# Optimization experiments

Hardware: AMD Instinct MI355X
Metric: run time of the kernel (lower is better)

The kernel has to match this reference:

```python
import jax, jax.numpy as jnp
import numpy as np

N, K = 50000, 10      # nodes, sampled neighbors (num_sample)
V, F = 200000, 128    # embedding table rows, input_dim
H = 64                # hidden per direction (hidden_dim=128, bidirectional)


def setup_inputs() -> dict:
    key = jax.random.key(0)
    ks = jax.random.split(key, 12)
    s = 1.0 / np.sqrt(H)  # torch LSTM init: U(-1/sqrt(H), 1/sqrt(H))
    u = lambda k, shape: jax.random.uniform(k, shape, jnp.float32, -s, s)
    return {
        "neigh_idx": jax.random.randint(ks[0], (N, K), 0, V),
        "embed_table": jax.random.normal(ks[1], (V, F), jnp.float32) * 0.02,
        # forward-direction LSTM params (torch gate order: i, f, g, o)
        "Wih_f": u(ks[2], (4 * H, F)), "Whh_f": u(ks[3], (4 * H, H)),
        "bih_f": u(ks[4], (4 * H,)),   "bhh_f": u(ks[5], (4 * H,)),
        # backward-direction LSTM params
        "Wih_b": u(ks[6], (4 * H, F)), "Whh_b": u(ks[7], (4 * H, H)),
        "bih_b": u(ks[8], (4 * H,)),   "bhh_b": u(ks[9], (4 * H,)),
    }


def _lstm_scan(x, Wih, Whh, bih, bhh):
    """x: [N,K,F] -> hidden outputs [N,K,H] (single direction)."""
    n = x.shape[0]
    # precompute input projections for all steps: [N,K,4H]
    xg = jnp.einsum('nkf,gf->nkg', x, Wih) + bih + bhh
    h0 = jnp.zeros((n, H), x.dtype)
    c0 = jnp.zeros((n, H), x.dtype)

    def step(carry, xt):
        h, c = carry
        gates = xt + h @ Whh.T
        i, f, g, o = jnp.split(gates, 4, axis=-1)
        i = jax.nn.sigmoid(i)
        f = jax.nn.sigmoid(f)
        g = jnp.tanh(g)
        o = jax.nn.sigmoid(o)
        c = f * c + i * g
        h = o * jnp.tanh(c)
        return (h, c), h

    _, hs = jax.lax.scan(step, (h0, c0), jnp.swapaxes(xg, 0, 1))  # [K,N,H]
    return jnp.swapaxes(hs, 0, 1)


def reference(neigh_idx, embed_table, Wih_f, Whh_f, bih_f, bhh_f,
              Wih_b, Whh_b, bih_b, bhh_b):
    x = embed_table[neigh_idx]  # gather: [N,K,F]
    # forward direction: last-step hidden
    h_f = _lstm_scan(x, Wih_f, Whh_f, bih_f, bhh_f)[:, -1, :]
    # backward direction processes reversed sequence; torch output[:, -1] of the
    # backward stream is its hidden after processing only element K-1 (step 0).
    h_b = _lstm_scan(x[:, ::-1, :], Wih_b, Whh_b, bih_b, bhh_b)[:, 0, :]
    return jnp.concatenate([h_f, h_b], axis=-1)  # [N, 2H]
```

## Files before the change

kernel.cpp:

```cpp
#include <hip/hip_runtime.h>
#include <hip/hip_bf16.h>


#define NN 50000
#define KK 10
#define FF 128
#define HH 64

#define WS_WIH_F 0
#define WS_WHH_F 32768
#define WS_WIH_B 49152

#define NPB 32
#define HS 72

typedef __bf16 bf16x8 __attribute__((ext_vector_type(8)));
typedef float f32x4 __attribute__((ext_vector_type(4)));

__device__ __forceinline__ float fast_sig(float x) {
    float e = exp2f(x * -1.44269504f);
    return __builtin_amdgcn_rcpf(1.0f + e);
}
__device__ __forceinline__ float fast_tanh(float x) {
    float xx = fminf(fmaxf(x, -15.0f), 15.0f);
    float e = exp2f(xx * 2.88539008f);
    return (e - 1.0f) * __builtin_amdgcn_rcpf(e + 1.0f);
}

__global__ void cvt_weights_kernel(const float* __restrict__ Wih_f,
                                   const float* __restrict__ Whh_f,
                                   const float* __restrict__ Wih_b,
                                   __bf16* __restrict__ ws) {
    int i = blockIdx.x * 256 + threadIdx.x;
    ws[WS_WIH_F + i] = (__bf16)Wih_f[i];
    if (i < 16384) ws[WS_WHH_F + i] = (__bf16)Whh_f[i];
    ws[WS_WIH_B + i] = (__bf16)Wih_b[i];
}

__global__ __launch_bounds__(256, 2) void lstm_agg_kernel(
    const int* __restrict__ nidx,
    const float* __restrict__ tab,
    const float* __restrict__ bih_f,
    const float* __restrict__ bhh_f,
    const float* __restrict__ bih_b,
    const float* __restrict__ bhh_b,
    const __bf16* __restrict__ ws,
    float* __restrict__ out)
{
    __shared__ float  x_lds[2][NPB * FF];
    __shared__ __bf16 h_lds[2][NPB * HS];
    __shared__ int    gq[NPB][KK];

    const int tid  = threadIdx.x;
    const int w    = tid >> 6;
    const int lane = tid & 63;
    const int q    = lane >> 4;
    const int c    = lane & 15;
    const int koff = q * 8;
    const int half = lane >> 5;
    const int l31  = lane & 31;
    const int node_base = blockIdx.x * NPB;
    const int sw = (c & 7) << 4;

    for (int i = tid; i < NPB * KK; i += 256) {
        int r = i / KK, k = i - r * KK;
        int node = min(node_base + r, NN - 1);
        gq[r][k] = nidx[node * KK + k];
    }

    auto stage = [&](int b, int kidx) {
#pragma unroll
        for (int j = 0; j < 4; ++j) {
            const int R = w * 8 + 2 * j + half;
            const int g = gq[R][kidx];
            const char* src = (const char*)tab + (size_t)g * 512
                              + ((l31 ^ (R & 7)) << 4);
            float* dst = &x_lds[b][(w * 8 + 2 * j) * FF];
            __builtin_amdgcn_global_load_lds(
                (const __attribute__((address_space(1))) void*)src,
                (__attribute__((address_space(3))) void*)dst, 16, 0, 0);
        }
    };

    __syncthreads();
    stage(0, 0);

    bf16x8 bWih[4][4], bWhh[4][2];
#pragma unroll
    for (int g = 0; g < 4; ++g) {
        int row = (g * 4 + w) * 16 + c;
#pragma unroll
        for (int kk = 0; kk < 4; ++kk)
            bWih[g][kk] = *(const bf16x8*)(ws + WS_WIH_F + row * FF + kk * 32 + koff);
#pragma unroll
        for (int kk = 0; kk < 2; ++kk)
            bWhh[g][kk] = *(const bf16x8*)(ws + WS_WHH_F + row * HH + kk * 32 + koff);
    }
    float bias[4];
#pragma unroll
    for (int g = 0; g < 4; ++g) {
        int u = g * 64 + w * 16 + c;
        bias[g] = bih_f[u] + bhh_f[u];
    }

    __syncthreads();

    f32x4 acc[4][2];
    float cst[2][4];
#pragma unroll
    for (int r = 0; r < 2; ++r)
#pragma unroll
        for (int e = 0; e < 4; ++e) cst[r][e] = 0.0f;

    for (int k = 0; k < KK; ++k) {
        const int cur = k & 1;
        if (k + 1 < KK) stage(cur ^ 1, k + 1);

#pragma unroll
        for (int g = 0; g < 4; ++g)
#pragma unroll
            for (int r = 0; r < 2; ++r)
                acc[g][r] = (f32x4){bias[g], bias[g], bias[g], bias[g]};

        const char* xb = (const char*)x_lds[cur];
#pragma unroll
        for (int r = 0; r < 2; ++r) {
            const char* rp = xb + (r * 16 + c) * 512;
            bf16x8 xa[4];
#pragma unroll
            for (int kk = 0; kk < 4; ++kk) {
                const int base = kk * 128 + q * 32;
                f32x4 lo = *(const f32x4*)(rp + ((base) ^ sw));
                f32x4 hi = *(const f32x4*)(rp + ((base + 16) ^ sw));
                bf16x8 v;
#pragma unroll
                for (int e = 0; e < 4; ++e) {
                    v[e]     = (__bf16)lo[e];
                    v[4 + e] = (__bf16)hi[e];
                }
                xa[kk] = v;
            }
#pragma unroll
            for (int g = 0; g < 4; ++g)
#pragma unroll
                for (int kk = 0; kk < 4; ++kk)
                    acc[g][r] = __builtin_amdgcn_mfma_f32_16x16x32_bf16(
                        xa[kk], bWih[g][kk], acc[g][r], 0, 0, 0);
        }

        if (k > 0) {
            const __bf16* hb = h_lds[(k - 1) & 1];
#pragma unroll
            for (int r = 0; r < 2; ++r) {
                bf16x8 ha[2];
#pragma unroll
                for (int kk = 0; kk < 2; ++kk)
                    ha[kk] = *(const bf16x8*)(hb + (r * 16 + c) * HS + kk * 32 + koff);
#pragma unroll
                for (int g = 0; g < 4; ++g)
#pragma unroll
                    for (int kk = 0; kk < 2; ++kk)
                        acc[g][r] = __builtin_amdgcn_mfma_f32_16x16x32_bf16(
                            ha[kk], bWhh[g][kk], acc[g][r], 0, 0, 0);
            }
        }

        const bool last = (k == KK - 1);
        __bf16* hw = h_lds[k & 1];
#pragma unroll
        for (int r = 0; r < 2; ++r)
#pragma unroll
            for (int reg = 0; reg < 4; ++reg) {
                float gi = fast_sig(acc[0][r][reg]);
                float gf = fast_sig(acc[1][r][reg]);
                float gg = fast_tanh(acc[2][r][reg]);
                float go = fast_sig(acc[3][r][reg]);
                float cn = gf * cst[r][reg] + gi * gg;
                cst[r][reg] = cn;
                float h = go * fast_tanh(cn);
                hw[(r * 16 + q * 4 + reg) * HS + w * 16 + c] = (__bf16)h;
                if (last) {
                    int node = node_base + r * 16 + q * 4 + reg;
                    if (node < NN) out[(size_t)node * 128 + w * 16 + c] = h;
                }
            }
        __syncthreads();
    }

    {
        const int gb[3] = {0, 2, 3};
        bf16x8 bW[3][4];
        float  bb[3];
#pragma unroll
        for (int j = 0; j < 3; ++j) {
            int row = (gb[j] * 4 + w) * 16 + c;
#pragma unroll
            for (int kk = 0; kk < 4; ++kk)
                bW[j][kk] = *(const bf16x8*)(ws + WS_WIH_B + row * FF + kk * 32 + koff);
            int u = gb[j] * 64 + w * 16 + c;
            bb[j] = bih_b[u] + bhh_b[u];
        }
        const char* xb = (const char*)x_lds[(KK - 1) & 1];
#pragma unroll
        for (int r = 0; r < 2; ++r) {
            f32x4 a0 = (f32x4){bb[0], bb[0], bb[0], bb[0]};
            f32x4 a1 = (f32x4){bb[1], bb[1], bb[1], bb[1]};
            f32x4 a2 = (f32x4){bb[2], bb[2], bb[2], bb[2]};
            const char* rp = xb + (r * 16 + c) * 512;
            bf16x8 xa[4];
#pragma unroll
            for (int kk = 0; kk < 4; ++kk) {
                const int base = kk * 128 + q * 32;
                f32x4 lo = *(const f32x4*)(rp + ((base) ^ sw));
                f32x4 hi = *(const f32x4*)(rp + ((base + 16) ^ sw));
                bf16x8 v;
#pragma unroll
                for (int e = 0; e < 4; ++e) {
                    v[e]     = (__bf16)lo[e];
                    v[4 + e] = (__bf16)hi[e];
                }
                xa[kk] = v;
            }
#pragma unroll
            for (int kk = 0; kk < 4; ++kk) {
                a0 = __builtin_amdgcn_mfma_f32_16x16x32_bf16(xa[kk], bW[0][kk], a0, 0, 0, 0);
                a1 = __builtin_amdgcn_mfma_f32_16x16x32_bf16(xa[kk], bW[1][kk], a1, 0, 0, 0);
                a2 = __builtin_amdgcn_mfma_f32_16x16x32_bf16(xa[kk], bW[2][kk], a2, 0, 0, 0);
            }
#pragma unroll
            for (int reg = 0; reg < 4; ++reg) {
                float gi = fast_sig(a0[reg]);
                float gg = fast_tanh(a1[reg]);
                float go = fast_sig(a2[reg]);
                float hb2 = go * fast_tanh(gi * gg);
                int node = node_base + r * 16 + q * 4 + reg;
                if (node < NN) out[(size_t)node * 128 + 64 + w * 16 + c] = hb2;
            }
        }
    }
}

extern "C" void kernel_launch(void* const* d_in, const int* in_sizes, int n_in,
                              void* d_out, int out_size, void* d_ws, size_t ws_size,
                              hipStream_t stream) {
    const int*   nidx  = (const int*)d_in[0];
    const float* tab   = (const float*)d_in[1];
    const float* Wih_f = (const float*)d_in[2];
    const float* Whh_f = (const float*)d_in[3];
    const float* bih_f = (const float*)d_in[4];
    const float* bhh_f = (const float*)d_in[5];
    const float* Wih_b = (const float*)d_in[6];
    const float* bih_b = (const float*)d_in[8];
    const float* bhh_b = (const float*)d_in[9];
    __bf16* ws  = (__bf16*)d_ws;
    float*  out = (float*)d_out;

    hipLaunchKernelGGL(cvt_weights_kernel, dim3(32768 / 256), dim3(256), 0, stream,
                       Wih_f, Whh_f, Wih_b, ws);

    const int blocks = (NN + NPB - 1) / NPB;
    hipLaunchKernelGGL(lstm_agg_kernel, dim3(blocks), dim3(256), 0, stream,
                       nidx, tab, bih_f, bhh_f, bih_b, bhh_b, ws, out);
}
```

Measured before the change: 274.7 us.

## Stage gathered embeddings through registers and store bf16 in LDS

Replaces the direct global-to-LDS async copy of fp32 embedding rows with register loads that are converted to bf16 once and written to a swizzled bf16 LDS buffer after the step's compute. This halves LDS footprint and read traffic, and removes the repeated fp32-to-bf16 conversion on every MFMA operand read, which may allow higher occupancy. In exchange the gather now holds 16 extra VGPRs across the step and needs explicit VALU stores, so load latency is hidden only by the compute between load and write.

```diff
diff --git a/kernel.cpp b/kernel.cpp
--- a/kernel.cpp
+++ b/kernel.cpp
@@ -47,7 +47,7 @@
     const __bf16* __restrict__ ws,
     float* __restrict__ out)
 {
-    __shared__ float  x_lds[2][NPB * FF];
+    __shared__ __bf16 x_lds[2][NPB * FF];
     __shared__ __bf16 h_lds[2][NPB * HS];
     __shared__ int    gq[NPB][KK];
 
@@ -57,10 +57,12 @@
     const int q    = lane >> 4;
     const int c    = lane & 15;
     const int koff = q * 8;
-    const int half = lane >> 5;
-    const int l31  = lane & 31;
     const int node_base = blockIdx.x * NPB;
     const int sw = (c & 7) << 4;
+
+    const int srow  = tid >> 3;
+    const int spart = tid & 7;
+    const int swW   = (srow & 7) << 4;
 
     for (int i = tid; i < NPB * KK; i += 256) {
         int r = i / KK, k = i - r * KK;
@@ -68,22 +70,28 @@
         gq[r][k] = nidx[node * KK + k];
     }
 
-    auto stage = [&](int b, int kidx) {
-#pragma unroll
-        for (int j = 0; j < 4; ++j) {
-            const int R = w * 8 + 2 * j + half;
-            const int g = gq[R][kidx];
-            const char* src = (const char*)tab + (size_t)g * 512
-                              + ((l31 ^ (R & 7)) << 4);
-            float* dst = &x_lds[b][(w * 8 + 2 * j) * FF];
-            __builtin_amdgcn_global_load_lds(
-                (const __attribute__((address_space(1))) void*)src,
-                (__attribute__((address_space(3))) void*)dst, 16, 0, 0);
-        }
+    f32x4 G[4];
+    auto stage_load = [&](int kidx) {
+        const float* src = tab + (size_t)gq[srow][kidx] * FF + spart * 16;
+#pragma unroll
+        for (int j = 0; j < 4; ++j) G[j] = *(const f32x4*)(src + j * 4);
     };
+    auto stage_write = [&](int b) {
+        bf16x8 v0, v1;
+#pragma unroll
+        for (int e = 0; e < 4; ++e) {
+            v0[e]     = (__bf16)G[0][e];
+            v0[4 + e] = (__bf16)G[1][e];
+            v1[e]     = (__bf16)G[2][e];
+            v1[4 + e] = (__bf16)G[3][e];
+        }
+        char* row = (char*)(x_lds[b] + srow * FF);
+        *(bf16x8*)(row + ((spart * 32)      ^ swW)) = v0;
+        *(bf16x8*)(row + ((spart * 32 + 16) ^ swW)) = v1;
+    };
 
     __syncthreads();
-    stage(0, 0);
+    stage_load(0);
 
     bf16x8 bWih[4][4], bWhh[4][2];
 #pragma unroll
@@ -103,6 +111,7 @@
         bias[g] = bih_f[u] + bhh_f[u];
     }
 
+    stage_write(0);
     __syncthreads();
 
     f32x4 acc[4][2];
@@ -114,7 +123,7 @@
 
     for (int k = 0; k < KK; ++k) {
         const int cur = k & 1;
-        if (k + 1 < KK) stage(cur ^ 1, k + 1);
+        if (k + 1 < KK) stage_load(k + 1);
 
 #pragma unroll
         for (int g = 0; g < 4; ++g)
@@ -125,21 +134,11 @@
         const char* xb = (const char*)x_lds[cur];
 #pragma unroll
         for (int r = 0; r < 2; ++r) {
-            const char* rp = xb + (r * 16 + c) * 512;
+            const char* rp = xb + (r * 16 + c) * 256;
             bf16x8 xa[4];
 #pragma unroll
-            for (int kk = 0; kk < 4; ++kk) {
-                const int base = kk * 128 + q * 32;
-                f32x4 lo = *(const f32x4*)(rp + ((base) ^ sw));
-                f32x4 hi = *(const f32x4*)(rp + ((base + 16) ^ sw));
-                bf16x8 v;
-#pragma unroll
-                for (int e = 0; e < 4; ++e) {
-                    v[e]     = (__bf16)lo[e];
-                    v[4 + e] = (__bf16)hi[e];
-                }
-                xa[kk] = v;
-            }
+            for (int kk = 0; kk < 4; ++kk)
+                xa[kk] = *(const bf16x8*)(rp + ((kk * 64 + q * 16) ^ sw));
 #pragma unroll
             for (int g = 0; g < 4; ++g)
 #pragma unroll
@@ -184,6 +183,8 @@
                     if (node < NN) out[(size_t)node * 128 + w * 16 + c] = h;
                 }
             }
+
+        if (k + 1 < KK) stage_write(cur ^ 1);
         __syncthreads();
     }
 
@@ -206,21 +207,11 @@
             f32x4 a0 = (f32x4){bb[0], bb[0], bb[0], bb[0]};
             f32x4 a1 = (f32x4){bb[1], bb[1], bb[1], bb[1]};
             f32x4 a2 = (f32x4){bb[2], bb[2], bb[2], bb[2]};
-            const char* rp = xb + (r * 16 + c) * 512;
+            const char* rp = xb + (r * 16 + c) * 256;
             bf16x8 xa[4];
 #pragma unroll
-            for (int kk = 0; kk < 4; ++kk) {
-                const int base = kk * 128 + q * 32;
-                f32x4 lo = *(const f32x4*)(rp + ((base) ^ sw));
-                f32x4 hi = *(const f32x4*)(rp + ((base + 16) ^ sw));
-                bf16x8 v;
-#pragma unroll
-                for (int e = 0; e < 4; ++e) {
-                    v[e]     = (__bf16)lo[e];
-                    v[4 + e] = (__bf16)hi[e];
-                }
-                xa[kk] = v;
-            }
+            for (int kk = 0; kk < 4; ++kk)
+                xa[kk] = *(const bf16x8*)(rp + ((kk * 64 + q * 16) ^ sw));
 #pragma unroll
             for (int kk = 0; kk < 4; ++kk) {
                 a0 = __builtin_amdgcn_mfma_f32_16x16x32_bf16(xa[kk], bW[0][kk], a0, 0, 0, 0);
```

Result: faster. 254.2 us (-7.5%).
